# Kernel tuning notes

Hardware: AMD Instinct MI355X
Metric: run time of the kernel (lower is better)

Reference implementation:

```python
import jax, jax.numpy as jnp
import numpy as np

B, T, C = 2, 2048, 2048
H = 16
D = C // H  # head_size = 128
ROPE_BASE = 10000.0


def _rope_cos_sin(seq_len, dim, dtype=jnp.float32):
    # torchtune RotaryPositionalEmbeddings: interleaved pair rotation
    inv_freq = 1.0 / (ROPE_BASE ** (jnp.arange(0, dim, 2, dtype=jnp.float32) / dim))  # [D/2]
    ang = jnp.arange(seq_len, dtype=jnp.float32)[:, None] * inv_freq[None, :]  # [T, D/2]
    return jnp.cos(ang).astype(dtype), jnp.sin(ang).astype(dtype)


def _apply_rope(x, cos, sin):
    # x: [B, T, H, D]; rotate interleaved pairs (even, odd)
    x1 = x[..., 0::2]
    x2 = x[..., 1::2]
    c = cos[None, :, None, :]
    s = sin[None, :, None, :]
    out = jnp.stack([x1 * c - x2 * s, x1 * s + x2 * c], axis=-1)  # [B,T,H,D/2,2]
    return out.reshape(x.shape)


def setup_inputs() -> dict:
    key = jax.random.key(0)
    ks = jax.random.split(key, 5)
    scale = 1.0 / np.sqrt(C)
    return {
        "x": jax.random.normal(ks[0], (B, T, C), jnp.float32),
        "W_attn": jax.random.normal(ks[1], (C, 3 * C), jnp.float32) * scale,
        "b_attn": jax.random.normal(ks[2], (3 * C,), jnp.float32) * 0.01,
        "W_proj": jax.random.normal(ks[3], (C, C), jnp.float32) * scale,
        "b_proj": jax.random.normal(ks[4], (C,), jnp.float32) * 0.01,
    }


def reference(x, W_attn, b_attn, W_proj, b_proj):
    b, t, c = x.shape
    qkv = x @ W_attn + b_attn                      # [B,T,3C]
    q, k, v = jnp.split(qkv, 3, axis=-1)
    q = q.reshape(b, t, H, D)
    k = k.reshape(b, t, H, D)
    v = v.reshape(b, t, H, D)
    cos, sin = _rope_cos_sin(t, D, x.dtype)
    q = _apply_rope(q, cos, sin)
    k = _apply_rope(k, cos, sin)
    # [B,H,T,D]
    q = q.transpose(0, 2, 1, 3)
    k = k.transpose(0, 2, 1, 3)
    v = v.transpose(0, 2, 1, 3)
    scores = jnp.einsum("bhqd,bhkd->bhqk", q, k) / jnp.sqrt(jnp.asarray(D, x.dtype))
    causal = jnp.tril(jnp.ones((t, t), dtype=bool))  # [T,T]
    scores = jnp.where(causal[None, None], scores, jnp.asarray(-jnp.inf, scores.dtype))
    probs = jax.nn.softmax(scores, axis=-1)
    out = jnp.einsum("bhqk,bhkd->bhqd", probs, v)  # [B,H,T,D]
    out = out.transpose(0, 2, 1, 3).reshape(b, t, c)
    return out @ W_proj + b_proj
```

## Files before the change

### kernel.cpp

```cpp
#include <hip/hip_runtime.h>
#include <hip/hip_bf16.h>
#include <math.h>

#define B_ 2
#define T_ 2048
#define C_ 2048
#define H_ 16
#define D_ 128
#define M_ (B_ * T_)
#define N3C (3 * C_)

typedef __attribute__((ext_vector_type(8))) short v8s;
typedef __attribute__((ext_vector_type(4))) float v4f;

typedef const __attribute__((address_space(1))) void* gas_t;
typedef __attribute__((address_space(3))) void* las_t;

__device__ __forceinline__ void gl16(const void* g, void* l) {
  __builtin_amdgcn_global_load_lds((gas_t)g, (las_t)l, 16, 0, 0);
}
__device__ __forceinline__ v8s ldv(const unsigned short* p) { return *(const v8s*)p; }

__device__ inline unsigned short f2bf(float f) {
  unsigned u = __builtin_bit_cast(unsigned, f);
  u += 0x7FFFu + ((u >> 16) & 1u);
  return (unsigned short)(u >> 16);
}
__device__ inline float bf2f(unsigned short h) {
  unsigned u = (unsigned)h << 16;
  return __builtin_bit_cast(float, u);
}

__global__ __launch_bounds__(256) void split_rows(
    const float* __restrict__ X, unsigned short* __restrict__ XH,
    unsigned short* __restrict__ XL) {
  const long i4 = ((long)blockIdx.x * 256 + threadIdx.x) * 4;
  float4 v = *(const float4*)(X + i4);
  ushort4 hh, ll;
  hh.x = f2bf(v.x); ll.x = f2bf(v.x - bf2f(hh.x));
  hh.y = f2bf(v.y); ll.y = f2bf(v.y - bf2f(hh.y));
  hh.z = f2bf(v.z); ll.z = f2bf(v.z - bf2f(hh.z));
  hh.w = f2bf(v.w); ll.w = f2bf(v.w - bf2f(hh.w));
  *(ushort4*)&XH[i4] = hh;
  *(ushort4*)&XL[i4] = ll;
}

__global__ __launch_bounds__(256) void convert_wT(
    const float* __restrict__ W, unsigned short* __restrict__ WH,
    unsigned short* __restrict__ WL, int K, int N) {
  __shared__ float Ts[64][68];
  const int tid = threadIdx.x;
  const int n0 = blockIdx.x * 64;
  const int k0 = blockIdx.y * 64;
#pragma unroll
  for (int it = 0; it < 4; ++it) {
    int f = it * 256 + tid;
    int r = f >> 4;
    int c4 = (f & 15) * 4;
    float4 v = *(const float4*)(W + (long)(k0 + r) * N + n0 + c4);
    *(float4*)&Ts[r][c4] = v;
  }
  __syncthreads();
#pragma unroll
  for (int it = 0; it < 4; ++it) {
    int f = it * 256 + tid;
    int rn = f >> 4;
    int c4 = (f & 15) * 4;
    float x0 = Ts[c4 + 0][rn];
    float x1 = Ts[c4 + 1][rn];
    float x2 = Ts[c4 + 2][rn];
    float x3 = Ts[c4 + 3][rn];
    ushort4 hh, ll;
    hh.x = f2bf(x0); ll.x = f2bf(x0 - bf2f(hh.x));
    hh.y = f2bf(x1); ll.y = f2bf(x1 - bf2f(hh.y));
    hh.z = f2bf(x2); ll.z = f2bf(x2 - bf2f(hh.z));
    hh.w = f2bf(x3); ll.w = f2bf(x3 - bf2f(hh.w));
    long o = (long)(n0 + rn) * K + k0 + c4;
    *(ushort4*)&WH[o] = hh;
    *(ushort4*)&WL[o] = ll;
  }
}

__global__ __launch_bounds__(256) void gemm_pre_mfma(
    const unsigned short* __restrict__ AH, const unsigned short* __restrict__ AL,
    const unsigned short* __restrict__ BH, const unsigned short* __restrict__ BL,
    const float* __restrict__ bias, float* __restrict__ C, int K, int N) {
  __shared__ unsigned short smem[2 * 4 * 4096];

  const int tid = threadIdx.x;
  const int lane = tid & 63;
  const int w = tid >> 6;
  const int lm = lane & 15;
  const int quad = lane >> 4;

  const int gx = gridDim.x;
  const int lin = blockIdx.y * gx + blockIdx.x;
  const int pid_m = (lin & 7) + ((lin >> 3) / gx) * 8;
  const int pid_n = (lin >> 3) % gx;
  const int bm = pid_m * 128;
  const int bn = pid_n * 128;

  const int wm = (w & 1) * 64;
  const int wn = (w >> 1) * 64;

  const int srow = 32 * w + (lane >> 2);
  const int scol = ((lane & 3) ^ ((lane >> 3) & 3)) * 8;
  const unsigned short* pAH0 = AH + (size_t)(bm + srow) * K + scol;
  const unsigned short* pAH1 = pAH0 + (size_t)16 * K;
  const unsigned short* pAL0 = AL + (size_t)(bm + srow) * K + scol;
  const unsigned short* pAL1 = pAL0 + (size_t)16 * K;
  const unsigned short* pBH0 = BH + (size_t)(bn + srow) * K + scol;
  const unsigned short* pBH1 = pBH0 + (size_t)16 * K;
  const unsigned short* pBL0 = BL + (size_t)(bn + srow) * K + scol;
  const unsigned short* pBL1 = pBL0 + (size_t)16 * K;

#define STAGE(base, kk) do {                                      \
    unsigned short* d_ = (base) + 1024 * w;                       \
    const int ko_ = (kk) * 32;                                    \
    gl16(pAH0 + ko_, d_);                                         \
    gl16(pAH1 + ko_, d_ + 512);                                   \
    gl16(pAL0 + ko_, d_ + 4096);                                  \
    gl16(pAL1 + ko_, d_ + 4096 + 512);                            \
    gl16(pBH0 + ko_, d_ + 8192);                                  \
    gl16(pBH1 + ko_, d_ + 8192 + 512);                            \
    gl16(pBL0 + ko_, d_ + 12288);                                 \
    gl16(pBL1 + ko_, d_ + 12288 + 512);                           \
  } while (0)

  v4f acc[4][4];
#pragma unroll
  for (int i = 0; i < 4; ++i)
#pragma unroll
    for (int j = 0; j < 4; ++j) {
      v4f z = {0.f, 0.f, 0.f, 0.f};
      acc[i][j] = z;
    }

  const int kswz = (quad ^ ((lm >> 1) & 3)) * 8;

  const int nk = K >> 5;
  unsigned short* sb = smem;
  unsigned short* nb = smem + 16384;

  STAGE(sb, 0);

  for (int t = 0; t < nk; ++t) {
    __syncthreads();

    if (t + 1 < nk) STAGE(nb, t + 1);

    const unsigned short* sAH = sb;
    const unsigned short* sAL = sb + 4096;
    const unsigned short* sBH = sb + 8192;
    const unsigned short* sBL = sb + 12288;

    v8s aH[4], aL[4], bHf[4], bLf[4];
#pragma unroll
    for (int mt = 0; mt < 4; ++mt) {
      const int r = wm + mt * 16 + lm;
      aH[mt] = *(const v8s*)&sAH[r * 32 + kswz];
      aL[mt] = *(const v8s*)&sAL[r * 32 + kswz];
    }
#pragma unroll
    for (int nt = 0; nt < 4; ++nt) {
      const int r = wn + nt * 16 + lm;
      bHf[nt] = *(const v8s*)&sBH[r * 32 + kswz];
      bLf[nt] = *(const v8s*)&sBL[r * 32 + kswz];
    }

    __builtin_amdgcn_s_setprio(1);
#pragma unroll
    for (int mt = 0; mt < 4; ++mt)
#pragma unroll
      for (int nt = 0; nt < 4; ++nt) {
        acc[mt][nt] = __builtin_amdgcn_mfma_f32_16x16x32_bf16(aH[mt], bHf[nt], acc[mt][nt], 0, 0, 0);
        acc[mt][nt] = __builtin_amdgcn_mfma_f32_16x16x32_bf16(aH[mt], bLf[nt], acc[mt][nt], 0, 0, 0);
        acc[mt][nt] = __builtin_amdgcn_mfma_f32_16x16x32_bf16(aL[mt], bHf[nt], acc[mt][nt], 0, 0, 0);
      }
    __builtin_amdgcn_s_setprio(0);

    unsigned short* tmp = sb; sb = nb; nb = tmp;
  }
#undef STAGE

  __syncthreads();
  float* eps = (float*)smem;
  float* myeps = eps + w * 1088;

  float bv[4];
#pragma unroll
  for (int nt = 0; nt < 4; ++nt) bv[nt] = bias[bn + wn + nt * 16 + lm];

  const int r2 = lane >> 2;
  const int c4 = (lane & 3) * 4;
#pragma unroll
  for (int mt = 0; mt < 4; ++mt) {
#pragma unroll
    for (int nt = 0; nt < 4; ++nt)
#pragma unroll
      for (int r = 0; r < 4; ++r)
        myeps[(quad * 4 + r) * 68 + nt * 16 + lm] = acc[mt][nt][r] + bv[nt];
    float* dst = C + (size_t)(bm + wm + mt * 16 + r2) * N + bn + wn + c4;
#pragma unroll
    for (int i = 0; i < 4; ++i) {
      float4 v = *(float4*)&myeps[r2 * 68 + c4 + i * 16];
      *(float4*)&dst[i * 16] = v;
    }
  }
}

#define BAR() do { asm volatile("" ::: "memory"); __builtin_amdgcn_s_barrier(); asm volatile("" ::: "memory"); } while (0)

__global__ __launch_bounds__(512, 2) void gemm_qkv_8ph(
    const unsigned short* __restrict__ AH, const unsigned short* __restrict__ AL,
    const unsigned short* __restrict__ BH, const unsigned short* __restrict__ BL,
    const float* __restrict__ bias, float* __restrict__ C, int K, int N) {
  __shared__ unsigned short smem[2 * 28672];

  const int tid = threadIdx.x;
  const int lane = tid & 63;
  const int w = tid >> 6;
  const int lm = lane & 15;
  const int quad = lane >> 4;

  const int gx = gridDim.x;
  const int lin = blockIdx.y * gx + blockIdx.x;
  const int pid_m = (lin & 7) + ((lin >> 3) / gx) * 8;
  const int pid_n = (lin >> 3) % gx;
  const int bm = pid_m * 256;
  const int bn = pid_n * 192;

  const int wm = (w & 1) * 128;
  const int wn = (w >> 1) * 48;

  const unsigned short* aS[4]; int aD[4];
#pragma unroll
  for (int j = 0; j < 4; ++j) {
    int g = tid + 512 * j;
    int pl = g >> 10;
    int p = g & 1023;
    int row = p >> 2;
    int c = (p & 3) ^ ((row >> 1) & 3);
    aS[j] = (pl ? AL : AH) + (size_t)(bm + row) * K + c * 8;
    aD[j] = pl * 8192 + p * 8;
  }
  const unsigned short* bS[3]; int bD[3];
#pragma unroll
  for (int j = 0; j < 3; ++j) {
    int g = tid + 512 * j;
    int pl = (g >= 768) ? 1 : 0;
    int p = g - pl * 768;
    int row = p >> 2;
    int c = (p & 3) ^ ((row >> 1) & 3);
    bS[j] = (pl ? BL : BH) + (size_t)(bn + row) * K + c * 8;
    bD[j] = 16384 + pl * 6144 + p * 8;
  }

  v4f acc[8][3];
#pragma unroll
  for (int i = 0; i < 8; ++i)
#pragma unroll
    for (int j = 0; j < 3; ++j) {
      v4f z = {0.f, 0.f, 0.f, 0.f};
      acc[i][j] = z;
    }

  const int kswz = (quad ^ ((lm >> 1) & 3)) * 8;
  const int nk = K >> 5;

#pragma unroll
  for (int j = 0; j < 4; ++j) gl16(aS[j], smem + aD[j]);
#pragma unroll
  for (int j = 0; j < 3; ++j) gl16(bS[j], smem + bD[j]);

#define MM3(MT, NT, AH_, AL_)                                                           \
  acc[MT][NT] = __builtin_amdgcn_mfma_f32_16x16x32_bf16(AH_, bh##NT, acc[MT][NT], 0, 0, 0); \
  acc[MT][NT] = __builtin_amdgcn_mfma_f32_16x16x32_bf16(AH_, bl##NT, acc[MT][NT], 0, 0, 0); \
  acc[MT][NT] = __builtin_amdgcn_mfma_f32_16x16x32_bf16(AL_, bh##NT, acc[MT][NT], 0, 0, 0);

#define DO_PHASE(MA, MB)                                                      \
  {                                                                           \
    v8s xh = ldv(sbuf + (wm + (MA) * 16 + lm) * 32 + kswz);                   \
    v8s xl = ldv(sbuf + 8192 + (wm + (MA) * 16 + lm) * 32 + kswz);            \
    v8s yh = ldv(sbuf + (wm + (MB) * 16 + lm) * 32 + kswz);                   \
    v8s yl = ldv(sbuf + 8192 + (wm + (MB) * 16 + lm) * 32 + kswz);            \
    BAR();                                                                    \
    __builtin_amdgcn_s_setprio(1);                                            \
    MM3(MA, 0, xh, xl) MM3(MA, 1, xh, xl) MM3(MA, 2, xh, xl)                  \
    MM3(MB, 0, yh, yl) MM3(MB, 1, yh, yl) MM3(MB, 2, yh, yl)                  \
    __builtin_amdgcn_s_setprio(0);                                            \
    BAR();                                                                    \
  }

  for (int t = 0; t < nk; ++t) {
    const unsigned short* sbuf = smem + (t & 1) * 28672;
    unsigned short* nbuf = (unsigned short*)smem + ((t + 1) & 1) * 28672;
    const int kn = (t + 1) * 32;
    const bool pf = (t + 1 < nk);

    if (pf) {
      gl16(aS[0] + kn, nbuf + aD[0]);
      gl16(aS[1] + kn, nbuf + aD[1]);
      gl16(aS[2] + kn, nbuf + aD[2]);
      gl16(aS[3] + kn, nbuf + aD[3]);
      gl16(bS[0] + kn, nbuf + bD[0]);
      gl16(bS[1] + kn, nbuf + bD[1]);
      gl16(bS[2] + kn, nbuf + bD[2]);
      asm volatile("s_waitcnt vmcnt(7)" ::: "memory");
    } else {
      asm volatile("s_waitcnt vmcnt(0)" ::: "memory");
    }
    BAR();

    v8s bh0 = ldv(sbuf + 16384 + (wn + lm) * 32 + kswz);
    v8s bl0 = ldv(sbuf + 22528 + (wn + lm) * 32 + kswz);
    v8s bh1 = ldv(sbuf + 16384 + (wn + 16 + lm) * 32 + kswz);
    v8s bl1 = ldv(sbuf + 22528 + (wn + 16 + lm) * 32 + kswz);
    v8s bh2 = ldv(sbuf + 16384 + (wn + 32 + lm) * 32 + kswz);
    v8s bl2 = ldv(sbuf + 22528 + (wn + 32 + lm) * 32 + kswz);
    {
      v8s xh = ldv(sbuf + (wm + 0 * 16 + lm) * 32 + kswz);
      v8s xl = ldv(sbuf + 8192 + (wm + 0 * 16 + lm) * 32 + kswz);
      v8s yh = ldv(sbuf + (wm + 1 * 16 + lm) * 32 + kswz);
      v8s yl = ldv(sbuf + 8192 + (wm + 1 * 16 + lm) * 32 + kswz);
      __builtin_amdgcn_s_setprio(1);
      MM3(0, 0, xh, xl) MM3(0, 1, xh, xl) MM3(0, 2, xh, xl)
      MM3(1, 0, yh, yl) MM3(1, 1, yh, yl) MM3(1, 2, yh, yl)
      __builtin_amdgcn_s_setprio(0);
      BAR();
    }
    DO_PHASE(2, 3)
    DO_PHASE(4, 5)
    DO_PHASE(6, 7)
  }
#undef DO_PHASE
#undef MM3

  __syncthreads();
  float* eps = (float*)smem;
  float* myeps = eps + w * 1088;

  float bv[3];
#pragma unroll
  for (int nt = 0; nt < 3; ++nt) bv[nt] = bias[bn + wn + nt * 16 + lm];

  const int r2 = lane >> 2;
  const int c4 = (lane & 3) * 4;
#pragma unroll
  for (int mt = 0; mt < 8; ++mt) {
#pragma unroll
    for (int nt = 0; nt < 3; ++nt)
#pragma unroll
      for (int r = 0; r < 4; ++r)
        myeps[(quad * 4 + r) * 68 + nt * 16 + lm] = acc[mt][nt][r] + bv[nt];
    float* dst = C + (size_t)(bm + wm + mt * 16 + r2) * N + bn + wn + c4;
#pragma unroll
    for (int i = 0; i < 3; ++i) {
      float4 v = *(float4*)&myeps[r2 * 68 + c4 + i * 16];
      *(float4*)&dst[i * 16] = v;
    }
  }
}

__global__ __launch_bounds__(256) void rope_split(
    const float* __restrict__ qkv,
    unsigned short* __restrict__ QH, unsigned short* __restrict__ QL,
    unsigned short* __restrict__ KH, unsigned short* __restrict__ KL,
    unsigned short* __restrict__ VTH, unsigned short* __restrict__ VTL) {
  const int tb = blockIdx.x;
  const int h = blockIdx.y;
  const int b = blockIdx.z;
  const int tid = threadIdx.x;

  __shared__ unsigned short VH_s[128][66];
  __shared__ unsigned short VL_s[128][66];

  for (int part = 0; part < 2; ++part) {
    unsigned short* OH = part ? KH : QH;
    unsigned short* OL = part ? KL : QL;
    const float sc = part ? 1.0f : 0.12751879523595298f;
    const size_t colbase = (size_t)part * C_ + (size_t)h * D_;
#pragma unroll 2
    for (int it = 0; it < 16; ++it) {
      int f = it * 256 + tid;
      int r = f >> 6;
      int i = f & 63;
      int t = tb * 64 + r;
      float inv = exp2f(-(float)i * (13.28771237954945f / 64.0f));
      float ang = (float)t * inv;
      float s, c;
      sincosf(ang, &s, &c);
      const float* src = qkv + (size_t)(b * T_ + t) * N3C + colbase + 2 * i;
      float2 x = *(const float2*)src;
      float ox = (x.x * c - x.y * s) * sc;
      float oy = (x.x * s + x.y * c) * sc;
      size_t dst = ((size_t)(b * H_ + h) * T_ + t) * D_ + 2 * i;
      unsigned short hx = f2bf(ox), hy = f2bf(oy);
      ushort2 hh; hh.x = hx; hh.y = hy;
      *(ushort2*)&OH[dst] = hh;
      ushort2 ll; ll.x = f2bf(ox - bf2f(hx)); ll.y = f2bf(oy - bf2f(hy));
      *(ushort2*)&OL[dst] = ll;
    }
  }

#pragma unroll
  for (int it = 0; it < 8; ++it) {
    int f = it * 256 + tid;
    int r = f >> 5;
    int d4 = (f & 31) * 4;
    float4 v = *(const float4*)(qkv + (size_t)(b * T_ + tb * 64 + r) * N3C + 2 * C_ + h * D_ + d4);
    float vv[4] = {v.x, v.y, v.z, v.w};
#pragma unroll
    for (int j = 0; j < 4; ++j) {
      unsigned short hi = f2bf(vv[j]);
      VH_s[d4 + j][r] = hi;
      VL_s[d4 + j][r] = f2bf(vv[j] - bf2f(hi));
    }
  }
  __syncthreads();
#pragma unroll
  for (int it = 0; it < 4; ++it) {
    int f = it * 256 + tid;
    int d = f >> 3;
    int c8 = (f & 7) * 8;
    size_t dst = ((size_t)(b * H_ + h) * D_ + d) * T_ + tb * 64 + c8;
    unsigned short th[8], tl[8];
#pragma unroll
    for (int j = 0; j < 8; ++j) { th[j] = VH_s[d][c8 + j]; tl[j] = VL_s[d][c8 + j]; }
    *(uint4*)&VTH[dst] = *(uint4*)th;
    *(uint4*)&VTL[dst] = *(uint4*)tl;
  }
}

__global__ __launch_bounds__(512, 4) void attn_mfma(
    const unsigned short* __restrict__ QH, const unsigned short* __restrict__ QL,
    const unsigned short* __restrict__ KH, const unsigned short* __restrict__ KL,
    const unsigned short* __restrict__ VTH, const unsigned short* __restrict__ VTL,
    unsigned short* __restrict__ OHp, unsigned short* __restrict__ OLp) {
  const int qb = (int)gridDim.x - 1 - (int)blockIdx.x;
  const int h = blockIdx.y;
  const int b = blockIdx.z;
  const int tid = threadIdx.x;
  const int lane = tid & 63;
  const int w = tid >> 6;
  const int lm = lane & 15;
  const int quad = lane >> 4;

  __shared__ unsigned short KS_H[32][136], KS_L[32][136];
  __shared__ unsigned short VS_H[128][40], VS_L[128][40];
  __shared__ unsigned short PS_H[128][40], PS_L[128][40];

  const size_t qbase = ((size_t)(b * H_ + h) * T_ + qb * 128 + w * 16 + lm) * D_;
  v8s qh[4], ql[4];
#pragma unroll
  for (int ks = 0; ks < 4; ++ks) {
    qh[ks] = *(const v8s*)&QH[qbase + ks * 32 + quad * 8];
    ql[ks] = *(const v8s*)&QL[qbase + ks * 32 + quad * 8];
  }

  v8s ones;
#pragma unroll
  for (int j = 0; j < 8; ++j) ones[j] = (short)0x3F80;

  const int kr = tid >> 4;
  const int kc = (tid & 15) * 8;
  const int vd = tid >> 2;
  const int vc = (tid & 3) * 8;

  const size_t kbase0 = (size_t)(b * H_ + h) * T_ * D_;
  const size_t vbase0 = (size_t)(b * H_ + h) * D_ * T_;
  const int nkb = 4 * qb + 4;

  uint4 khp = *(const uint4*)&KH[kbase0 + (size_t)kr * D_ + kc];
  uint4 klp = *(const uint4*)&KL[kbase0 + (size_t)kr * D_ + kc];
  uint4 vhp = *(const uint4*)&VTH[vbase0 + (size_t)vd * T_ + vc];
  uint4 vlp = *(const uint4*)&VTL[vbase0 + (size_t)vd * T_ + vc];

  v4f acc_o[8], acc_l;
#pragma unroll
  for (int nt = 0; nt < 8; ++nt) {
    v4f z = {0.f, 0.f, 0.f, 0.f};
    acc_o[nt] = z;
  }
  {
    v4f z = {0.f, 0.f, 0.f, 0.f};
    acc_l = z;
  }

  const float M2 = 32.0f;

  for (int kb = 0; kb < nkb; ++kb) {
    __syncthreads();
    *(uint4*)&KS_H[kr][kc] = khp;
    *(uint4*)&KS_L[kr][kc] = klp;
    *(uint4*)&VS_H[vd][vc] = vhp;
    *(uint4*)&VS_L[vd][vc] = vlp;
    __syncthreads();

    if (kb + 1 < nkb) {
      size_t kg = kbase0 + (size_t)((kb + 1) * 32 + kr) * D_ + kc;
      khp = *(const uint4*)&KH[kg];
      klp = *(const uint4*)&KL[kg];
      size_t vg = vbase0 + (size_t)vd * T_ + (kb + 1) * 32 + vc;
      vhp = *(const uint4*)&VTH[vg];
      vlp = *(const uint4*)&VTL[vg];
    }

    v4f s0, s1;
    {
      v4f z = {0.f, 0.f, 0.f, 0.f};
      s0 = z; s1 = z;
    }
#pragma unroll
    for (int ks = 0; ks < 4; ++ks) {
      int k8 = ks * 32 + quad * 8;
      v8s bh0 = *(const v8s*)&KS_H[lm][k8];
      v8s bl0 = *(const v8s*)&KS_L[lm][k8];
      v8s bh1 = *(const v8s*)&KS_H[16 + lm][k8];
      v8s bl1 = *(const v8s*)&KS_L[16 + lm][k8];
      s0 = __builtin_amdgcn_mfma_f32_16x16x32_bf16(qh[ks], bh0, s0, 0, 0, 0);
      s1 = __builtin_amdgcn_mfma_f32_16x16x32_bf16(qh[ks], bh1, s1, 0, 0, 0);
      s0 = __builtin_amdgcn_mfma_f32_16x16x32_bf16(qh[ks], bl0, s0, 0, 0, 0);
      s1 = __builtin_amdgcn_mfma_f32_16x16x32_bf16(qh[ks], bl1, s1, 0, 0, 0);
      s0 = __builtin_amdgcn_mfma_f32_16x16x32_bf16(ql[ks], bh0, s0, 0, 0, 0);
      s1 = __builtin_amdgcn_mfma_f32_16x16x32_bf16(ql[ks], bh1, s1, 0, 0, 0);
    }

#pragma unroll
    for (int r = 0; r < 4; ++r) {
      int rowg = qb * 128 + w * 16 + quad * 4 + r;
      float v0 = (kb * 32 + lm > rowg) ? -INFINITY : s0[r];
      float v1 = (kb * 32 + 16 + lm > rowg) ? -INFINITY : s1[r];
      float p0 = __builtin_amdgcn_exp2f(v0 - M2);
      float p1 = __builtin_amdgcn_exp2f(v1 - M2);

      int prow = w * 16 + quad * 4 + r;
      unsigned short p0h = f2bf(p0);
      PS_H[prow][lm] = p0h;
      PS_L[prow][lm] = f2bf(p0 - bf2f(p0h));
      unsigned short p1h = f2bf(p1);
      PS_H[prow][16 + lm] = p1h;
      PS_L[prow][16 + lm] = f2bf(p1 - bf2f(p1h));
    }

    v8s ph = *(const v8s*)&PS_H[w * 16 + lm][quad * 8];
    v8s pl = *(const v8s*)&PS_L[w * 16 + lm][quad * 8];
    acc_l = __builtin_amdgcn_mfma_f32_16x16x32_bf16(ph, ones, acc_l, 0, 0, 0);
    acc_l = __builtin_amdgcn_mfma_f32_16x16x32_bf16(pl, ones, acc_l, 0, 0, 0);
#pragma unroll
    for (int nt = 0; nt < 8; ++nt) {
      v8s vh = *(const v8s*)&VS_H[nt * 16 + lm][quad * 8];
      v8s vl = *(const v8s*)&VS_L[nt * 16 + lm][quad * 8];
      acc_o[nt] = __builtin_amdgcn_mfma_f32_16x16x32_bf16(ph, vh, acc_o[nt], 0, 0, 0);
      acc_o[nt] = __builtin_amdgcn_mfma_f32_16x16x32_bf16(ph, vl, acc_o[nt], 0, 0, 0);
      acc_o[nt] = __builtin_amdgcn_mfma_f32_16x16x32_bf16(pl, vh, acc_o[nt], 0, 0, 0);
    }
  }

#pragma unroll
  for (int r = 0; r < 4; ++r) {
    float invl = 1.0f / acc_l[r];
    size_t row = (size_t)(b * T_ + qb * 128 + w * 16 + quad * 4 + r);
#pragma unroll
    for (int nt = 0; nt < 8; ++nt) {
      float o = acc_o[nt][r] * invl;
      unsigned short oh = f2bf(o);
      size_t idx = row * C_ + h * D_ + nt * 16 + lm;
      OHp[idx] = oh;
      OLp[idx] = f2bf(o - bf2f(oh));
    }
  }
}

extern "C" void kernel_launch(void* const* d_in, const int* in_sizes, int n_in,
                              void* d_out, int out_size, void* d_ws, size_t ws_size,
                              hipStream_t stream) {
  const float* x      = (const float*)d_in[0];
  const float* W_attn = (const float*)d_in[1];
  const float* b_attn = (const float*)d_in[2];
  const float* W_proj = (const float*)d_in[3];
  const float* b_proj = (const float*)d_in[4];
  float* out = (float*)d_out;

  char* wsb = (char*)d_ws;
  const size_t MiB = 1048576;
  float* qkv = (float*)wsb;
  unsigned short* WtaH = (unsigned short*)(wsb + 96 * MiB);
  unsigned short* WtaL = (unsigned short*)(wsb + 120 * MiB);
  unsigned short* XH   = (unsigned short*)(wsb + 144 * MiB);
  unsigned short* XL   = (unsigned short*)(wsb + 160 * MiB);
  unsigned short* QH   = (unsigned short*)(wsb + 96 * MiB);
  unsigned short* QL   = (unsigned short*)(wsb + 112 * MiB);
  unsigned short* KH   = (unsigned short*)(wsb + 128 * MiB);
  unsigned short* KL   = (unsigned short*)(wsb + 144 * MiB);
  unsigned short* VTH  = (unsigned short*)(wsb + 160 * MiB);
  unsigned short* VTL  = (unsigned short*)(wsb + 176 * MiB);
  unsigned short* WtpH = (unsigned short*)(wsb + 32 * MiB);
  unsigned short* WtpL = (unsigned short*)(wsb + 40 * MiB);
  unsigned short* AOH  = (unsigned short*)(wsb + 48 * MiB);
  unsigned short* AOL  = (unsigned short*)(wsb + 64 * MiB);

  convert_wT<<<dim3(N3C / 64, C_ / 64), 256, 0, stream>>>(W_attn, WtaH, WtaL, C_, N3C);
  split_rows<<<dim3((M_ * C_) / 1024), 256, 0, stream>>>(x, XH, XL);
  gemm_qkv_8ph<<<dim3(N3C / 192, M_ / 256), 512, 0, stream>>>(
      XH, XL, WtaH, WtaL, b_attn, qkv, C_, N3C);
  rope_split<<<dim3(T_ / 64, H_, B_), 256, 0, stream>>>(qkv, QH, QL, KH, KL, VTH, VTL);
  convert_wT<<<dim3(C_ / 64, C_ / 64), 256, 0, stream>>>(W_proj, WtpH, WtpL, C_, C_);
  attn_mfma<<<dim3(T_ / 128, H_, B_), 512, 0, stream>>>(
      QH, QL, KH, KL, VTH, VTL, AOH, AOL);
  gemm_pre_mfma<<<dim3(C_ / 128, M_ / 128), 256, 0, stream>>>(
      AOH, AOL, WtpH, WtpL, b_proj, out, C_, C_);
}
```

Baseline: 722.5 us.

## Split A-tile prefetch into halves interleaved with MFMA phases, fewer barriers

```diff
diff --git a/kernel.cpp b/kernel.cpp
--- a/kernel.cpp
+++ b/kernel.cpp
@@ -234,15 +234,18 @@
   const int wn = (w >> 1) * 48;
 
   const unsigned short* aS[4]; int aD[4];
-#pragma unroll
-  for (int j = 0; j < 4; ++j) {
-    int g = tid + 512 * j;
-    int pl = g >> 10;
-    int p = g & 1023;
-    int row = p >> 2;
-    int c = (p & 3) ^ ((row >> 1) & 3);
-    aS[j] = (pl ? AL : AH) + (size_t)(bm + row) * K + c * 8;
-    aD[j] = pl * 8192 + p * 8;
+  {
+    const int seg = tid >> 8;
+    const int rr = (tid & 255) >> 2;
+    const int cc = tid & 3;
+#pragma unroll
+    for (int j = 0; j < 4; ++j) {
+      int row = (j >> 1) * 64 + seg * 128 + rr;
+      int pl = j & 1;
+      int c = cc ^ ((row >> 1) & 3);
+      aS[j] = (pl ? AL : AH) + (size_t)(bm + row) * K + c * 8;
+      aD[j] = pl * 8192 + row * 32 + cc * 8;
+    }
   }
   const unsigned short* bS[3]; int bD[3];
 #pragma unroll
@@ -268,29 +271,21 @@
   const int kswz = (quad ^ ((lm >> 1) & 3)) * 8;
   const int nk = K >> 5;
 
-#pragma unroll
-  for (int j = 0; j < 4; ++j) gl16(aS[j], smem + aD[j]);
-#pragma unroll
-  for (int j = 0; j < 3; ++j) gl16(bS[j], smem + bD[j]);
+  gl16(bS[0], smem + bD[0]);
+  gl16(bS[1], smem + bD[1]);
+  gl16(bS[2], smem + bD[2]);
+  gl16(aS[0], smem + aD[0]);
+  gl16(aS[1], smem + aD[1]);
+  gl16(aS[2], smem + aD[2]);
+  gl16(aS[3], smem + aD[3]);
 
 #define MM3(MT, NT, AH_, AL_)                                                           \
   acc[MT][NT] = __builtin_amdgcn_mfma_f32_16x16x32_bf16(AH_, bh##NT, acc[MT][NT], 0, 0, 0); \
   acc[MT][NT] = __builtin_amdgcn_mfma_f32_16x16x32_bf16(AH_, bl##NT, acc[MT][NT], 0, 0, 0); \
   acc[MT][NT] = __builtin_amdgcn_mfma_f32_16x16x32_bf16(AL_, bh##NT, acc[MT][NT], 0, 0, 0);
-
-#define DO_PHASE(MA, MB)                                                      \
-  {                                                                           \
-    v8s xh = ldv(sbuf + (wm + (MA) * 16 + lm) * 32 + kswz);                   \
-    v8s xl = ldv(sbuf + 8192 + (wm + (MA) * 16 + lm) * 32 + kswz);            \
-    v8s yh = ldv(sbuf + (wm + (MB) * 16 + lm) * 32 + kswz);                   \
-    v8s yl = ldv(sbuf + 8192 + (wm + (MB) * 16 + lm) * 32 + kswz);            \
-    BAR();                                                                    \
-    __builtin_amdgcn_s_setprio(1);                                            \
-    MM3(MA, 0, xh, xl) MM3(MA, 1, xh, xl) MM3(MA, 2, xh, xl)                  \
-    MM3(MB, 0, yh, yl) MM3(MB, 1, yh, yl) MM3(MB, 2, yh, yl)                  \
-    __builtin_amdgcn_s_setprio(0);                                            \
-    BAR();                                                                    \
-  }
+#define MROW(MT, XH_, XL_) MM3(MT, 0, XH_, XL_) MM3(MT, 1, XH_, XL_) MM3(MT, 2, XH_, XL_)
+#define AFRAG(MT) ldv(sbuf + (wm + (MT) * 16 + lm) * 32 + kswz)
+#define AFRAGL(MT) ldv(sbuf + 8192 + (wm + (MT) * 16 + lm) * 32 + kswz)
 
   for (int t = 0; t < nk; ++t) {
     const unsigned short* sbuf = smem + (t & 1) * 28672;
@@ -299,16 +294,12 @@
     const bool pf = (t + 1 < nk);
 
     if (pf) {
-      gl16(aS[0] + kn, nbuf + aD[0]);
-      gl16(aS[1] + kn, nbuf + aD[1]);
-      gl16(aS[2] + kn, nbuf + aD[2]);
-      gl16(aS[3] + kn, nbuf + aD[3]);
       gl16(bS[0] + kn, nbuf + bD[0]);
       gl16(bS[1] + kn, nbuf + bD[1]);
       gl16(bS[2] + kn, nbuf + bD[2]);
-      asm volatile("s_waitcnt vmcnt(7)" ::: "memory");
+      asm volatile("s_waitcnt vmcnt(5)" ::: "memory");
     } else {
-      asm volatile("s_waitcnt vmcnt(0)" ::: "memory");
+      asm volatile("s_waitcnt vmcnt(2)" ::: "memory");
     }
     BAR();
 
@@ -319,21 +310,50 @@
     v8s bh2 = ldv(sbuf + 16384 + (wn + 32 + lm) * 32 + kswz);
     v8s bl2 = ldv(sbuf + 22528 + (wn + 32 + lm) * 32 + kswz);
     {
-      v8s xh = ldv(sbuf + (wm + 0 * 16 + lm) * 32 + kswz);
-      v8s xl = ldv(sbuf + 8192 + (wm + 0 * 16 + lm) * 32 + kswz);
-      v8s yh = ldv(sbuf + (wm + 1 * 16 + lm) * 32 + kswz);
-      v8s yl = ldv(sbuf + 8192 + (wm + 1 * 16 + lm) * 32 + kswz);
+      v8s x0h = AFRAG(0), x0l = AFRAGL(0);
+      v8s x1h = AFRAG(1), x1l = AFRAGL(1);
+      v8s x2h = AFRAG(2), x2l = AFRAGL(2);
+      v8s x3h = AFRAG(3), x3l = AFRAGL(3);
       __builtin_amdgcn_s_setprio(1);
-      MM3(0, 0, xh, xl) MM3(0, 1, xh, xl) MM3(0, 2, xh, xl)
-      MM3(1, 0, yh, yl) MM3(1, 1, yh, yl) MM3(1, 2, yh, yl)
+      MROW(0, x0h, x0l)
+      MROW(1, x1h, x1l)
       __builtin_amdgcn_s_setprio(0);
-      BAR();
-    }
-    DO_PHASE(2, 3)
-    DO_PHASE(4, 5)
-    DO_PHASE(6, 7)
-  }
-#undef DO_PHASE
+      if (pf) {
+        gl16(aS[0] + kn, nbuf + aD[0]);
+        gl16(aS[1] + kn, nbuf + aD[1]);
+      }
+      __builtin_amdgcn_s_setprio(1);
+      MROW(2, x2h, x2l)
+      MROW(3, x3h, x3l)
+      __builtin_amdgcn_s_setprio(0);
+    }
+
+    if (pf) {
+      gl16(aS[2] + kn, nbuf + aD[2]);
+      gl16(aS[3] + kn, nbuf + aD[3]);
+      asm volatile("s_waitcnt vmcnt(7)" ::: "memory");
+    } else {
+      asm volatile("s_waitcnt vmcnt(0)" ::: "memory");
+    }
+    BAR();
+
+    {
+      v8s x4h = AFRAG(4), x4l = AFRAGL(4);
+      v8s x5h = AFRAG(5), x5l = AFRAGL(5);
+      v8s x6h = AFRAG(6), x6l = AFRAGL(6);
+      v8s x7h = AFRAG(7), x7l = AFRAGL(7);
+      __builtin_amdgcn_s_setprio(1);
+      MROW(4, x4h, x4l)
+      MROW(5, x5h, x5l)
+      MROW(6, x6h, x6l)
+      MROW(7, x7h, x7l)
+      __builtin_amdgcn_s_setprio(0);
+    }
+    BAR();
+  }
+#undef AFRAGL
+#undef AFRAG
+#undef MROW
 #undef MM3
 
   __syncthreads();
```

Measured after the change: 711.8 us. No clear change (-1.5%).
